# Kernel optimization log

Hardware: AMD Instinct MI355X
Metric: run time of the kernel (lower is better)

The kernel has to match this reference:

```python
import jax, jax.numpy as jnp
import numpy as np

DIM = 1024
S_SIZE = 512
M_SIZE = 4096
L_SIZE = 8192
MERGE_THRESHOLD = 0.98
L_ALPHA = 0.1
K_PROMOTE = max(1, S_SIZE // 4)  # torch: min(len(candidates), max(1, s_size//4)); candidates >> s_size here


def _l2norm(x, axis=-1):
    # F.normalize(p=2) with eps clamp
    return x / jnp.maximum(jnp.linalg.norm(x, axis=axis, keepdims=True), 1e-12)


def _update(processed_tokens, s_memory, m_memory, l_memory, m_utility, l_utility, wq, bq, wk, bk, s_ptr):
    cand = processed_tokens.reshape(-1, DIM)
    # --- S tier: scatter top-k-norm candidates into ring buffer (vectorized; K<=S so slots distinct) ---
    norms = jnp.linalg.norm(cand, axis=1)
    _, top_idx = jax.lax.top_k(norms, K_PROMOTE)
    pos = (s_ptr + jnp.arange(K_PROMOTE)) % S_SIZE
    s_mem = s_memory.at[pos].set(cand[top_idx])
    s_ptr_new = (s_ptr + K_PROMOTE) % S_SIZE
    # --- promotion attention (1 head, only attn weights used): pick best short-term slot ---
    q = l_memory.mean(axis=0) @ wq.T + bq                      # [dim]
    kproj = s_mem @ wk.T + bk                                  # [S, dim]
    attn = jax.nn.softmax(kproj @ q / jnp.sqrt(jnp.asarray(DIM, cand.dtype)))
    best_s_idx = jnp.argmax(attn)
    candidate = s_mem[best_s_idx]                              # [dim]

    # --- M tier: promote / merge / replace ---
    def not_full(mm, mu):
        ridx = jnp.argmin(mu)
        return mm.at[ridx].set(candidate), mu.at[ridx].set(mu.mean() + 1e-5)

    def full(mm, mu):
        mm_norm = _l2norm(mm)
        sims = mm_norm @ _l2norm(candidate)                    # [M]
        msi = jnp.argmax(sims)
        sim_cand = sims[msi]

        def merge_with_candidate(mm, mu):
            merged = _l2norm((mm[msi] + candidate) / 2.0)
            return mm.at[msi].set(merged), mu.at[msi].set((mu[msi] + mu.mean()) / 2.0)

        def try_internal_merge(mm, mu):
            # most redundant pair: strict lower triangle of cosine sim matrix
            sim_mat = mm_norm @ mm_norm.T                      # [M, M]
            sim_mat = jnp.where(jnp.triu(jnp.ones((M_SIZE, M_SIZE), bool)), -1.0, sim_mat)
            flat = jnp.argmax(sim_mat)
            internal_sim = sim_mat.reshape(-1)[flat]
            idx1, idx2 = flat // M_SIZE, flat % M_SIZE

            def do_pair_merge(mm, mu):
                merged = _l2norm((mm[idx1] + mm[idx2]) / 2.0)
                mm2 = mm.at[idx1].set(merged).at[idx2].set(candidate)
                mu1 = mu.at[idx1].set((mu[idx1] + mu[idx2]) / 2.0)
                mu2 = mu1.at[idx2].set(mu1.mean() + 1e-5)      # torch recomputes mean after idx1 write
                return mm2, mu2

            def replace_weakest(mm, mu):
                li = jnp.argmin(mu)
                stronger = jnp.linalg.norm(candidate) > jnp.linalg.norm(mm[li])
                mm2 = jnp.where(stronger, mm.at[li].set(candidate), mm)
                mu2 = jnp.where(stronger, mu.at[li].set(mu.mean() + 1e-5), mu)
                return mm2, mu2

            return jax.lax.cond(internal_sim > MERGE_THRESHOLD, do_pair_merge, replace_weakest, mm, mu)

        return jax.lax.cond(sim_cand > MERGE_THRESHOLD, merge_with_candidate, try_internal_merge, mm, mu)

    is_m_full = ~jnp.any(m_utility == 0)
    m_mem, m_util = jax.lax.cond(is_m_full, full, not_full, m_memory, m_utility)
    # --- L tier: consolidate most-used M slot into least-used L slot ---
    mi = jnp.argmax(m_util)
    lj = jnp.argmin(l_utility)
    consolidated = (1.0 - L_ALPHA) * l_memory[lj] + L_ALPHA * m_mem[mi]
    l_mem = l_memory.at[lj].set(consolidated)
    l_util = l_utility.at[lj].set(l_utility.mean())            # mean of pre-write values
    return s_mem, m_mem, l_mem, m_util, l_util, s_ptr_new


def setup_inputs() -> dict:
    key = jax.random.key(0)
    ks = jax.random.split(key, 10)
    scale = 1.0 / np.sqrt(DIM)
    return {
        "processed_tokens": jax.random.normal(ks[0], (4, 4096, DIM), jnp.float32),
        "s_memory": jax.random.normal(ks[1], (S_SIZE, DIM), jnp.float32),
        "m_memory": jax.random.normal(ks[2], (M_SIZE, DIM), jnp.float32),
        "l_memory": jax.random.normal(ks[3], (L_SIZE, DIM), jnp.float32),
        "m_utility": jax.random.uniform(ks[4], (M_SIZE,), jnp.float32) + 0.01,  # >0 -> 'm full' branch
        "l_utility": jax.random.uniform(ks[5], (L_SIZE,), jnp.float32) + 0.01,
        "wq": jax.random.normal(ks[6], (DIM, DIM), jnp.float32) * scale,
        "bq": jnp.zeros((DIM,), jnp.float32),
        "wk": jax.random.normal(ks[7], (DIM, DIM), jnp.float32) * scale,
        "bk": jnp.zeros((DIM,), jnp.float32),
        "s_ptr": 0,
    }


def reference(processed_tokens, s_memory, m_memory, l_memory, m_utility, l_utility, wq, bq, wk, bk, s_ptr):
    return _update(processed_tokens, s_memory, m_memory, l_memory, m_utility, l_utility, wq, bq, wk, bk, s_ptr)
```

## Files before the change

kernel.cpp:

```cpp
#include <hip/hip_runtime.h>

#define DIMV 1024
#define SSZ 512
#define MSZ 4096
#define LSZ 8192
#define KPROM 128
#define NCAND 16384

typedef __attribute__((ext_vector_type(4))) float f32x4;
typedef __attribute__((ext_vector_type(4))) unsigned int u32x4;
typedef __attribute__((ext_vector_type(4))) unsigned short u16x4;
typedef __attribute__((ext_vector_type(8))) __bf16 bf16x8;

#define OUT_S 0ull
#define OUT_M 524288ull
#define OUT_L 4718592ull
#define OUT_MU 13107200ull
#define OUT_LU 13111296ull
#define OUT_SPTR 13119488ull

#define SC_BF16 0ull
#define SC_NORMS 2100000ull
#define SC_TOPIDX 2117000ull
#define SC_LPART 2120000ull
#define SC_LMEAN 2260000ull
#define SC_Q 2262000ull
#define SC_RPART 2270000ull
#define SC_R 2410000ull
#define SC_CSCAL 2412000ull
#define SC_LOGITS 2413000ull
#define SC_BEST 2414000ull
#define SC_MNORM 2415000ull
#define SC_SIMS 2420000ull
#define SC_PPV 2425000ull
#define SC_PPI 2426000ull
#define SC_DEC 2427000ull

__device__ __forceinline__ float wave_sum(float v) {
#pragma unroll
  for (int o = 32; o > 0; o >>= 1) v += __shfl_down(v, o, 64);
  return v;
}
__device__ __forceinline__ int wave_sum_i(int v) {
#pragma unroll
  for (int o = 32; o > 0; o >>= 1) v += __shfl_down(v, o, 64);
  return v;
}
__device__ __forceinline__ void wave_maxidx(float& v, int& i) {
#pragma unroll
  for (int o = 32; o > 0; o >>= 1) {
    float ov = __shfl_down(v, o, 64);
    int oi = __shfl_down(i, o, 64);
    if (ov > v || (ov == v && oi < i)) { v = ov; i = oi; }
  }
}
__device__ __forceinline__ void wave_minidx(float& v, int& i) {
#pragma unroll
  for (int o = 32; o > 0; o >>= 1) {
    float ov = __shfl_down(v, o, 64);
    int oi = __shfl_down(i, o, 64);
    if (ov < v || (ov == v && oi < i)) { v = ov; i = oi; }
  }
}
__device__ __forceinline__ unsigned short f2bf(float x) {
  unsigned u = __float_as_uint(x);
  return (unsigned short)((u + 0x7FFFu + ((u >> 16) & 1u)) >> 16);
}

__global__ void k_cand_norms(const float* __restrict__ cand, float* __restrict__ norms) {
  int lane = threadIdx.x & 63, w = threadIdx.x >> 6;
  int row = blockIdx.x * 4 + w;
  const f32x4* p = (const f32x4*)(cand + (size_t)row * DIMV);
  float s = 0.f;
#pragma unroll
  for (int c = 0; c < 4; ++c) {
    f32x4 v = p[c * 64 + lane];
    s += v.x * v.x + v.y * v.y + v.z * v.z + v.w * v.w;
  }
  s = wave_sum(s);
  if (lane == 0) norms[row] = sqrtf(s);
}

__device__ int scan_excl_1024(int v, int* sh, int* total) {
  int t = threadIdx.x;
  sh[t] = v;
  __syncthreads();
  for (int o = 1; o < 1024; o <<= 1) {
    int x = (t >= o) ? sh[t - o] : 0;
    __syncthreads();
    sh[t] += x;
    __syncthreads();
  }
  int incl = sh[t];
  *total = sh[1023];
  __syncthreads();
  return incl - v;
}

__global__ void k_topk(const float* __restrict__ norms, int* __restrict__ topidx) {
  __shared__ int sh[1024];
  __shared__ int s_w[16];
  __shared__ int s_tot;
  __shared__ unsigned s_selkey[KPROM];
  __shared__ int s_selidx[KPROM];
  int t = threadIdx.x, lane = t & 63, w = t >> 6;
  unsigned key[16];
#pragma unroll
  for (int j = 0; j < 16; ++j) key[j] = __float_as_uint(norms[t * 16 + j]);

  unsigned prefix = 0;
  int remaining = KPROM;
  for (int bit = 31; bit >= 0; --bit) {
    unsigned himask = (bit == 31) ? 0u : (0xFFFFFFFFu << (bit + 1));
    int c = 0;
#pragma unroll
    for (int j = 0; j < 16; ++j)
      c += (((key[j] & himask) == prefix) && ((key[j] >> bit) & 1u)) ? 1 : 0;
    c = wave_sum_i(c);
    if (lane == 0) s_w[w] = c;
    __syncthreads();
    if (t == 0) {
      int tot = 0;
      for (int i = 0; i < 16; ++i) tot += s_w[i];
      s_tot = tot;
    }
    __syncthreads();
    int tot = s_tot;
    __syncthreads();
    if (tot >= remaining) prefix |= (1u << bit);
    else remaining -= tot;
  }
  unsigned T = prefix;

  int cgt = 0, ceq = 0;
#pragma unroll
  for (int j = 0; j < 16; ++j) { cgt += (key[j] > T); ceq += (key[j] == T); }
  int total_gt, total_eq;
  int sgt = scan_excl_1024(cgt, sh, &total_gt);
  int seq = scan_excl_1024(ceq, sh, &total_eq);
  int need_eq = KPROM - total_gt;
  int g = sgt, e = seq;
#pragma unroll
  for (int j = 0; j < 16; ++j) {
    if (key[j] > T) { s_selkey[g] = key[j]; s_selidx[g] = t * 16 + j; ++g; }
    else if (key[j] == T) {
      if (e < need_eq) { s_selkey[total_gt + e] = key[j]; s_selidx[total_gt + e] = t * 16 + j; }
      ++e;
    }
  }
  __syncthreads();
  if (t < KPROM) {
    unsigned mk = s_selkey[t];
    int mi = s_selidx[t];
    int rank = 0;
    for (int q2 = 0; q2 < KPROM; ++q2) {
      unsigned qk = s_selkey[q2];
      int qi = s_selidx[q2];
      rank += (qk > mk || (qk == mk && qi < mi)) ? 1 : 0;
    }
    topidx[rank] = mi;
  }
}

__global__ void k_write_s(const float* __restrict__ cand, const float* __restrict__ s_memory,
                          const int* __restrict__ topidx, const int* __restrict__ s_ptr,
                          float* __restrict__ out_s, float* __restrict__ out_sptr) {
  int r = blockIdx.x;
  int sp = s_ptr[0];
  int k = (r - sp + SSZ) & (SSZ - 1);
  const float* src = (k < KPROM) ? (cand + (size_t)topidx[k] * DIMV) : (s_memory + (size_t)r * DIMV);
  ((f32x4*)(out_s + (size_t)r * DIMV))[threadIdx.x] = ((const f32x4*)src)[threadIdx.x];
  if (r == 0 && threadIdx.x == 0) out_sptr[0] = (float)((sp + KPROM) % SSZ);
}

__global__ void k_lpart(const float* __restrict__ l_memory, float* __restrict__ lpart) {
  int b = blockIdx.x, t = threadIdx.x;
  f32x4 a = {0.f, 0.f, 0.f, 0.f};
  const f32x4* base = (const f32x4*)(l_memory + (size_t)b * 64 * DIMV);
  for (int r = 0; r < 64; ++r) a += base[r * 256 + t];
  ((f32x4*)(lpart + (size_t)b * DIMV))[t] = a;
}
__global__ void k_lmean(const float* __restrict__ lpart, float* __restrict__ lmean) {
  int c = threadIdx.x;
  f32x4 a = {0.f, 0.f, 0.f, 0.f};
  for (int p = 0; p < 128; ++p) a += ((const f32x4*)lpart)[p * 256 + c];
  ((f32x4*)lmean)[c] = a * (1.f / 8192.f);
}

__global__ void k_q(const float* __restrict__ wq, const float* __restrict__ bq,
                    const float* __restrict__ lmean, float* __restrict__ qv) {
  int lane = threadIdx.x & 63, w = threadIdx.x >> 6;
  int d = blockIdx.x * 4 + w;
  const f32x4* row = (const f32x4*)(wq + (size_t)d * DIMV);
  const f32x4* lm = (const f32x4*)lmean;
  float s = 0.f;
#pragma unroll
  for (int c = 0; c < 4; ++c) {
    f32x4 a = row[c * 64 + lane], b = lm[c * 64 + lane];
    s += a.x * b.x + a.y * b.y + a.z * b.z + a.w * b.w;
  }
  s = wave_sum(s);
  if (lane == 0) qv[d] = s + bq[d];
}

__global__ void k_rpart(const float* __restrict__ wk, const float* __restrict__ qv, float* __restrict__ rpart) {
  int b = blockIdx.x, t = threadIdx.x;
  f32x4 a = {0.f, 0.f, 0.f, 0.f};
  for (int r = 0; r < 8; ++r) {
    float qd = qv[b * 8 + r];
    f32x4 v = ((const f32x4*)(wk + (size_t)(b * 8 + r) * DIMV))[t];
    a += v * qd;
  }
  ((f32x4*)(rpart + (size_t)b * DIMV))[t] = a;
}
__global__ void k_rfinal(const float* __restrict__ rpart, float* __restrict__ rv) {
  int c = threadIdx.x;
  f32x4 a = {0.f, 0.f, 0.f, 0.f};
  for (int p = 0; p < 128; ++p) a += ((const f32x4*)rpart)[p * 256 + c];
  ((f32x4*)rv)[c] = a;
}
__global__ void k_cscal(const float* __restrict__ bk, const float* __restrict__ qv, float* __restrict__ cs) {
  __shared__ float sw[4];
  int lane = threadIdx.x & 63, w = threadIdx.x >> 6;
  f32x4 a = ((const f32x4*)bk)[threadIdx.x];
  f32x4 b = ((const f32x4*)qv)[threadIdx.x];
  float s = a.x * b.x + a.y * b.y + a.z * b.z + a.w * b.w;
  s = wave_sum(s);
  if (lane == 0) sw[w] = s;
  __syncthreads();
  if (threadIdx.x == 0) cs[0] = sw[0] + sw[1] + sw[2] + sw[3];
}

__global__ void k_logits(const float* __restrict__ out_s, const float* __restrict__ rv,
                         const float* __restrict__ cs, float* __restrict__ logits) {
  int lane = threadIdx.x & 63, w = threadIdx.x >> 6;
  int srow = blockIdx.x * 4 + w;
  const f32x4* a = (const f32x4*)(out_s + (size_t)srow * DIMV);
  const f32x4* b = (const f32x4*)rv;
  float s = 0.f;
#pragma unroll
  for (int c = 0; c < 4; ++c) {
    f32x4 x = a[c * 64 + lane], y = b[c * 64 + lane];
    s += x.x * y.x + x.y * y.y + x.z * y.z + x.w * y.w;
  }
  s = wave_sum(s);
  if (lane == 0) logits[srow] = s + cs[0];
}

__global__ void k_argmax_logits(const float* __restrict__ logits, const float* __restrict__ out_s,
                                int* __restrict__ best, float* __restrict__ cnorm) {
  __shared__ float swv[4];
  __shared__ int swi[4];
  int t = threadIdx.x, lane = t & 63, w = t >> 6;
  float v0 = logits[t], v1 = logits[t + 256];
  float bv;
  int bidx;
  if (v1 > v0) { bv = v1; bidx = t + 256; } else { bv = v0; bidx = t; }
  wave_maxidx(bv, bidx);
  if (lane == 0) { swv[w] = bv; swi[w] = bidx; }
  __syncthreads();
  if (t == 0) {
    float a = swv[0]; int ai = swi[0];
    for (int i = 1; i < 4; ++i)
      if (swv[i] > a || (swv[i] == a && swi[i] < ai)) { a = swv[i]; ai = swi[i]; }
    best[0] = ai;
  }
  __syncthreads();
  int bi = best[0];
  f32x4 c4 = ((const f32x4*)(out_s + (size_t)bi * DIMV))[t];
  float s = c4.x * c4.x + c4.y * c4.y + c4.z * c4.z + c4.w * c4.w;
  s = wave_sum(s);
  __syncthreads();
  if (lane == 0) swv[w] = s;
  __syncthreads();
  if (t == 0) cnorm[0] = sqrtf(swv[0] + swv[1] + swv[2] + swv[3]);
}

__global__ void k_msims(const float* __restrict__ m, const float* __restrict__ out_s,
                        const int* __restrict__ best, const float* __restrict__ cnorm,
                        unsigned short* __restrict__ mb, float* __restrict__ mnorm,
                        float* __restrict__ sims) {
  int lane = threadIdx.x & 63, w = threadIdx.x >> 6;
  int row = blockIdx.x * 4 + w;
  const f32x4* mp = (const f32x4*)(m + (size_t)row * DIMV);
  const f32x4* cp = (const f32x4*)(out_s + (size_t)best[0] * DIMV);
  float ss = 0.f, sd = 0.f;
#pragma unroll
  for (int c = 0; c < 4; ++c) {
    int i = c * 64 + lane;
    f32x4 v = mp[i], u = cp[i];
    ss += v.x * v.x + v.y * v.y + v.z * v.z + v.w * v.w;
    sd += v.x * u.x + v.y * u.y + v.z * u.z + v.w * u.w;
    u16x4 h;
    h.x = f2bf(v.x); h.y = f2bf(v.y); h.z = f2bf(v.z); h.w = f2bf(v.w);
    ((u16x4*)(mb + (size_t)row * DIMV))[i] = h;
  }
  ss = wave_sum(ss);
  sd = wave_sum(sd);
  if (lane == 0) {
    float n = sqrtf(ss);
    mnorm[row] = n;
    sims[row] = sd / (fmaxf(n, 1e-12f) * fmaxf(cnorm[0], 1e-12f));
  }
}

__global__ __launch_bounds__(256) void k_pairmax(const unsigned short* __restrict__ mb,
                                                 const float* __restrict__ mnorm,
                                                 float* __restrict__ pv, int* __restrict__ pidx) {
  __shared__ unsigned short At[128 * 72];
  __shared__ unsigned short Bt[128 * 72];
  __shared__ float spv[4];
  __shared__ int spi[4];
  int b = blockIdx.x;
  int bi = 0, acc0 = 0;
  while (acc0 + bi + 1 <= b) { acc0 += bi + 1; ++bi; }
  int bj = b - acc0;
  int t = threadIdx.x, lane = t & 63, w = t >> 6;
  int wr = w >> 1, wc = w & 1;
  int rl = lane & 15, kq = (lane >> 4) * 8, riq = (lane >> 4) * 4;
  int rowA0 = bi * 128, rowB0 = bj * 128;

  f32x4 acc[4][4];
  f32x4 z = {0.f, 0.f, 0.f, 0.f};
#pragma unroll
  for (int i = 0; i < 4; ++i)
#pragma unroll
    for (int j = 0; j < 4; ++j) acc[i][j] = z;

  for (int kc = 0; kc < DIMV; kc += 64) {
    __syncthreads();
#pragma unroll
    for (int c = 0; c < 4; ++c) {
      int chunk = c * 256 + t;
      int r = chunk >> 3, co = (chunk & 7) * 8;
      u32x4 va = *(const u32x4*)(mb + (size_t)(rowA0 + r) * DIMV + kc + co);
      u32x4 vb = *(const u32x4*)(mb + (size_t)(rowB0 + r) * DIMV + kc + co);
      *(u32x4*)(At + r * 72 + co) = va;
      *(u32x4*)(Bt + r * 72 + co) = vb;
    }
    __syncthreads();
#pragma unroll
    for (int ks = 0; ks < 64; ks += 32) {
      bf16x8 af[4], bfv[4];
#pragma unroll
      for (int ti = 0; ti < 4; ++ti)
        af[ti] = *(const bf16x8*)(At + (wr * 64 + ti * 16 + rl) * 72 + ks + kq);
#pragma unroll
      for (int tj = 0; tj < 4; ++tj)
        bfv[tj] = *(const bf16x8*)(Bt + (wc * 64 + tj * 16 + rl) * 72 + ks + kq);
#pragma unroll
      for (int ti = 0; ti < 4; ++ti)
#pragma unroll
        for (int tj = 0; tj < 4; ++tj)
          acc[ti][tj] = __builtin_amdgcn_mfma_f32_16x16x32_bf16(af[ti], bfv[tj], acc[ti][tj], 0, 0, 0);
    }
  }
  float ni[16], nj[4];
#pragma unroll
  for (int ti = 0; ti < 4; ++ti)
#pragma unroll
    for (int r = 0; r < 4; ++r)
      ni[ti * 4 + r] = fmaxf(mnorm[rowA0 + wr * 64 + ti * 16 + riq + r], 1e-12f);
#pragma unroll
  for (int tj = 0; tj < 4; ++tj)
    nj[tj] = fmaxf(mnorm[rowB0 + wc * 64 + tj * 16 + rl], 1e-12f);

  float bv = -3.402823466e38f;
  int bidx = 0x7FFFFFFF;
#pragma unroll
  for (int ti = 0; ti < 4; ++ti)
#pragma unroll
    for (int tj = 0; tj < 4; ++tj)
#pragma unroll
      for (int r = 0; r < 4; ++r) {
        int gi = rowA0 + wr * 64 + ti * 16 + riq + r;
        int gj = rowB0 + wc * 64 + tj * 16 + rl;
        if (gi > gj) {
          float s = acc[ti][tj][r] / (ni[ti * 4 + r] * nj[tj]);
          int fi = gi * MSZ + gj;
          if (s > bv || (s == bv && fi < bidx)) { bv = s; bidx = fi; }
        }
      }
  wave_maxidx(bv, bidx);
  if (lane == 0) { spv[w] = bv; spi[w] = bidx; }
  __syncthreads();
  if (t == 0) {
    float a = spv[0]; int ai = spi[0];
    for (int i = 1; i < 4; ++i)
      if (spv[i] > a || (spv[i] == a && spi[i] < ai)) { a = spv[i]; ai = spi[i]; }
    pv[b] = a;
    pidx[b] = ai;
  }
}

__global__ void k_decide(const float* __restrict__ pv, const int* __restrict__ pidx,
                         const float* __restrict__ sims, const float* __restrict__ mu,
                         const float* __restrict__ mnorm, const float* __restrict__ cnorm,
                         int nblk, int* __restrict__ dec_i, float* __restrict__ dec_f) {
  __shared__ float swv[4];
  __shared__ int swi[4];
  __shared__ float ssum[4];
  __shared__ int szf[4];
  __shared__ float s_res[2];
  __shared__ int s_resi[2];
  int t = threadIdx.x, lane = t & 63, w = t >> 6;

  float bv = -3.402823466e38f;
  int bidx = 0x7FFFFFFF;
  for (int i = t; i < nblk; i += 256) {
    float v = pv[i];
    int fi = pidx[i];
    if (v > bv || (v == bv && fi < bidx)) { bv = v; bidx = fi; }
  }
  wave_maxidx(bv, bidx);
  if (lane == 0) { swv[w] = bv; swi[w] = bidx; }
  __syncthreads();
  if (t == 0) {
    float a = swv[0]; int ai = swi[0];
    for (int i = 1; i < 4; ++i)
      if (swv[i] > a || (swv[i] == a && swi[i] < ai)) { a = swv[i]; ai = swi[i]; }
    s_res[0] = a; s_resi[0] = ai;
  }
  __syncthreads();

  bv = -3.402823466e38f;
  bidx = 0x7FFFFFFF;
#pragma unroll
  for (int j = 0; j < 16; ++j) {
    int i = t * 16 + j;
    float v = sims[i];
    if (v > bv) { bv = v; bidx = i; }
  }
  wave_maxidx(bv, bidx);
  if (lane == 0) { swv[w] = bv; swi[w] = bidx; }
  __syncthreads();
  if (t == 0) {
    float a = swv[0]; int ai = swi[0];
    for (int i = 1; i < 4; ++i)
      if (swv[i] > a || (swv[i] == a && swi[i] < ai)) { a = swv[i]; ai = swi[i]; }
    s_res[1] = a; s_resi[1] = ai;
  }
  __syncthreads();

  float sum = 0.f, mnv = 3.402823466e38f;
  int mni = 0x7FFFFFFF, zf = 0;
#pragma unroll
  for (int j = 0; j < 16; ++j) {
    int i = t * 16 + j;
    float v = mu[i];
    sum += v;
    if (v < mnv) { mnv = v; mni = i; }
    if (v == 0.f) zf = 1;
  }
  sum = wave_sum(sum);
  wave_minidx(mnv, mni);
#pragma unroll
  for (int o = 32; o > 0; o >>= 1) zf |= __shfl_down(zf, o, 64);
  if (lane == 0) { ssum[w] = sum; swv[w] = mnv; swi[w] = mni; szf[w] = zf; }
  __syncthreads();
  if (t == 0) {
    float muSum = ssum[0] + ssum[1] + ssum[2] + ssum[3];
    float a = swv[0]; int li = swi[0];
    for (int i = 1; i < 4; ++i)
      if (swv[i] < a || (swv[i] == a && swi[i] < li)) { a = swv[i]; li = swi[i]; }
    int anyz = szf[0] | szf[1] | szf[2] | szf[3];
    float muMean = muSum / 4096.f;
    float internal_sim = s_res[0];
    int iflat = s_resi[0];
    float sim_cand = s_res[1];
    int msi = s_resi[1];
    int branch, i1 = -1, i2 = -1;
    float u1 = 0.f, u2 = 0.f;
    if (anyz) {
      branch = 0; i1 = li; u1 = muMean + 1e-5f;
    } else if (sim_cand > 0.98f) {
      branch = 1; i1 = msi; u1 = (mu[msi] + muMean) * 0.5f;
    } else if (internal_sim > 0.98f) {
      branch = 2; i1 = iflat / MSZ; i2 = iflat - (iflat / MSZ) * MSZ;
      float o1 = mu[i1], o2 = mu[i2];
      u1 = (o1 + o2) * 0.5f;
      u2 = (muSum - o1 + u1) / 4096.f + 1e-5f;
    } else {
      if (cnorm[0] > mnorm[li]) { branch = 0; i1 = li; u1 = muMean + 1e-5f; }
      else branch = 4;
    }
    dec_i[0] = branch; dec_i[1] = i1; dec_i[2] = i2;
    dec_f[0] = u1; dec_f[1] = u2;
  }
}

__global__ void k_write_m(const float* __restrict__ m, const float* __restrict__ out_s,
                          const int* __restrict__ best, const int* __restrict__ dec_i,
                          float* __restrict__ out_m) {
  __shared__ float sred[4];
  int row = blockIdx.x, t = threadIdx.x, lane = t & 63, w = t >> 6;
  int branch = dec_i[0], i1 = dec_i[1], i2 = dec_i[2];
  int mode = 0;
  if ((branch == 0 && row == i1) || (branch == 2 && row == i2)) mode = 1;
  else if (branch == 1 && row == i1) mode = 2;
  else if (branch == 2 && row == i1) mode = 3;
  f32x4* dst = (f32x4*)(out_m + (size_t)row * DIMV);
  if (mode == 0) {
    dst[t] = ((const f32x4*)(m + (size_t)row * DIMV))[t];
  } else if (mode == 1) {
    dst[t] = ((const f32x4*)(out_s + (size_t)best[0] * DIMV))[t];
  } else {
    f32x4 a = ((const f32x4*)(m + (size_t)row * DIMV))[t];
    f32x4 bb = (mode == 2) ? ((const f32x4*)(out_s + (size_t)best[0] * DIMV))[t]
                           : ((const f32x4*)(m + (size_t)i2 * DIMV))[t];
    f32x4 v = (a + bb) * 0.5f;
    float ss = v.x * v.x + v.y * v.y + v.z * v.z + v.w * v.w;
    ss = wave_sum(ss);
    if (lane == 0) sred[w] = ss;
    __syncthreads();
    float nrm = fmaxf(sqrtf(sred[0] + sred[1] + sred[2] + sred[3]), 1e-12f);
    dst[t] = v / nrm;
  }
}

__global__ void k_write_mu(const float* __restrict__ mu, const int* __restrict__ dec_i,
                           const float* __restrict__ dec_f, float* __restrict__ out_mu) {
  int i = blockIdx.x * 256 + threadIdx.x;
  float v = mu[i];
  int branch = dec_i[0];
  if (branch != 4 && i == dec_i[1]) v = dec_f[0];
  if (branch == 2 && i == dec_i[2]) v = dec_f[1];
  out_mu[i] = v;
}

__global__ void k_ltier(const float* __restrict__ out_mu, const float* __restrict__ lu,
                        float* __restrict__ out_lu, int* __restrict__ wsi) {
  __shared__ float swv[4];
  __shared__ int swi[4];
  __shared__ float ssum[4];
  __shared__ float s_mean;
  __shared__ int s_lj;
  int t = threadIdx.x, lane = t & 63, w = t >> 6;
  float bv = -3.402823466e38f;
  int bidx = 0x7FFFFFFF;
#pragma unroll
  for (int j = 0; j < 16; ++j) {
    int i = t * 16 + j;
    float v = out_mu[i];
    if (v > bv) { bv = v; bidx = i; }
  }
  wave_maxidx(bv, bidx);
  if (lane == 0) { swv[w] = bv; swi[w] = bidx; }
  __syncthreads();
  if (t == 0) {
    float a = swv[0]; int ai = swi[0];
    for (int i = 1; i < 4; ++i)
      if (swv[i] > a || (swv[i] == a && swi[i] < ai)) { a = swv[i]; ai = swi[i]; }
    wsi[1] = ai;
  }
  __syncthreads();
  float mnv = 3.402823466e38f, sum = 0.f;
  int mni = 0x7FFFFFFF;
#pragma unroll
  for (int j = 0; j < 32; ++j) {
    int i = t * 32 + j;
    float v = lu[i];
    sum += v;
    if (v < mnv) { mnv = v; mni = i; }
  }
  sum = wave_sum(sum);
  wave_minidx(mnv, mni);
  if (lane == 0) { swv[w] = mnv; swi[w] = mni; ssum[w] = sum; }
  __syncthreads();
  if (t == 0) {
    float a = swv[0]; int ai = swi[0];
    for (int i = 1; i < 4; ++i)
      if (swv[i] < a || (swv[i] == a && swi[i] < ai)) { a = swv[i]; ai = swi[i]; }
    s_lj = ai;
    s_mean = (ssum[0] + ssum[1] + ssum[2] + ssum[3]) / 8192.f;
    wsi[0] = ai;
  }
  __syncthreads();
  int lj = s_lj;
  float lmv = s_mean;
#pragma unroll
  for (int j = 0; j < 32; ++j) {
    int i = t * 32 + j;
    out_lu[i] = (i == lj) ? lmv : lu[i];
  }
}

__global__ void k_write_l(const float* __restrict__ l_memory, const float* __restrict__ out_m,
                          const int* __restrict__ wsi, float* __restrict__ out_l) {
  int row = blockIdx.x, t = threadIdx.x;
  int lj = wsi[0], mi = wsi[1];
  f32x4 v = ((const f32x4*)(l_memory + (size_t)row * DIMV))[t];
  if (row == lj) {
    f32x4 mv = ((const f32x4*)(out_m + (size_t)mi * DIMV))[t];
    v = v * 0.9f + mv * 0.1f;
  }
  ((f32x4*)(out_l + (size_t)row * DIMV))[t] = v;
}

extern "C" void kernel_launch(void* const* d_in, const int* in_sizes, int n_in,
                              void* d_out, int out_size, void* d_ws, size_t ws_size,
                              hipStream_t stream) {
  const float* cand = (const float*)d_in[0];
  const float* s_memory = (const float*)d_in[1];
  const float* m_memory = (const float*)d_in[2];
  const float* l_memory = (const float*)d_in[3];
  const float* m_utility = (const float*)d_in[4];
  const float* l_utility = (const float*)d_in[5];
  const float* wq = (const float*)d_in[6];
  const float* bq = (const float*)d_in[7];
  const float* wk = (const float*)d_in[8];
  const float* bk = (const float*)d_in[9];
  const int* s_ptr = (const int*)d_in[10];

  float* out = (float*)d_out;
  float* out_s = out + OUT_S;
  float* out_m = out + OUT_M;
  float* out_l = out + OUT_L;
  float* out_mu = out + OUT_MU;
  float* out_lu = out + OUT_LU;
  float* out_sptr = out + OUT_SPTR;

  float* lsc = out_l;
  unsigned short* mb = (unsigned short*)(lsc + SC_BF16);
  float* norms = lsc + SC_NORMS;
  int* topidx = (int*)(lsc + SC_TOPIDX);
  float* lpart = lsc + SC_LPART;
  float* lmean = lsc + SC_LMEAN;
  float* qv = lsc + SC_Q;
  float* rpart = lsc + SC_RPART;
  float* rv = lsc + SC_R;
  float* cs = lsc + SC_CSCAL;
  float* logits = lsc + SC_LOGITS;
  int* best = (int*)(lsc + SC_BEST);
  float* cnorm = lsc + SC_BEST + 1;
  float* mnorm = lsc + SC_MNORM;
  float* sims = lsc + SC_SIMS;
  float* pv = lsc + SC_PPV;
  int* pidx = (int*)(lsc + SC_PPI);
  int* dec_i = (int*)(lsc + SC_DEC);
  float* dec_f = lsc + SC_DEC + 4;
  int* wsi = (int*)d_ws;

  k_cand_norms<<<4096, 256, 0, stream>>>(cand, norms);
  k_topk<<<1, 1024, 0, stream>>>(norms, topidx);
  k_write_s<<<512, 256, 0, stream>>>(cand, s_memory, topidx, s_ptr, out_s, out_sptr);
  k_lpart<<<128, 256, 0, stream>>>(l_memory, lpart);
  k_lmean<<<1, 256, 0, stream>>>(lpart, lmean);
  k_q<<<256, 256, 0, stream>>>(wq, bq, lmean, qv);
  k_rpart<<<128, 256, 0, stream>>>(wk, qv, rpart);
  k_rfinal<<<1, 256, 0, stream>>>(rpart, rv);
  k_cscal<<<1, 256, 0, stream>>>(bk, qv, cs);
  k_logits<<<128, 256, 0, stream>>>(out_s, rv, cs, logits);
  k_argmax_logits<<<1, 256, 0, stream>>>(logits, out_s, best, cnorm);
  k_msims<<<1024, 256, 0, stream>>>(m_memory, out_s, best, cnorm, mb, mnorm, sims);
  k_pairmax<<<528, 256, 0, stream>>>(mb, mnorm, pv, pidx);
  k_decide<<<1, 256, 0, stream>>>(pv, pidx, sims, m_utility, mnorm, cnorm, 528, dec_i, dec_f);
  k_write_m<<<4096, 256, 0, stream>>>(m_memory, out_s, best, dec_i, out_m);
  k_write_mu<<<16, 256, 0, stream>>>(m_utility, dec_i, dec_f, out_mu);
  k_ltier<<<1, 256, 0, stream>>>(out_mu, l_utility, out_lu, wsi);
  k_write_l<<<8192, 256, 0, stream>>>(l_memory, out_m, wsi, out_l);
}
```

Baseline: 332.1 us.

## Merge launch chain into fewer multi-role kernels and retile pair-similarity GEMM

New measurement: 327.0 us. No clear change (-1.5%).

```diff
diff --git a/kernel.cpp b/kernel.cpp
--- a/kernel.cpp
+++ b/kernel.cpp
@@ -6,6 +6,7 @@
 #define LSZ 8192
 #define KPROM 128
 #define NCAND 16384
+#define NPAIR 1056
 
 typedef __attribute__((ext_vector_type(4))) float f32x4;
 typedef __attribute__((ext_vector_type(4))) unsigned int u32x4;
@@ -23,25 +24,17 @@
 #define SC_NORMS 2100000ull
 #define SC_TOPIDX 2117000ull
 #define SC_LPART 2120000ull
-#define SC_LMEAN 2260000ull
-#define SC_Q 2262000ull
-#define SC_RPART 2270000ull
-#define SC_R 2410000ull
-#define SC_CSCAL 2412000ull
+#define SC_RV 2260000ull
+#define SC_LMEAN 2262000ull
+#define SC_Q 2264000ull
 #define SC_LOGITS 2413000ull
 #define SC_BEST 2414000ull
 #define SC_MNORM 2415000ull
 #define SC_SIMS 2420000ull
 #define SC_PPV 2425000ull
-#define SC_PPI 2426000ull
-#define SC_DEC 2427000ull
+#define SC_PPI 2427000ull
 
 __device__ __forceinline__ float wave_sum(float v) {
-#pragma unroll
-  for (int o = 32; o > 0; o >>= 1) v += __shfl_down(v, o, 64);
-  return v;
-}
-__device__ __forceinline__ int wave_sum_i(int v) {
 #pragma unroll
   for (int o = 32; o > 0; o >>= 1) v += __shfl_down(v, o, 64);
   return v;
@@ -67,18 +60,44 @@
   return (unsigned short)((u + 0x7FFFu + ((u >> 16) & 1u)) >> 16);
 }
 
-__global__ void k_cand_norms(const float* __restrict__ cand, float* __restrict__ norms) {
-  int lane = threadIdx.x & 63, w = threadIdx.x >> 6;
-  int row = blockIdx.x * 4 + w;
-  const f32x4* p = (const f32x4*)(cand + (size_t)row * DIMV);
-  float s = 0.f;
-#pragma unroll
-  for (int c = 0; c < 4; ++c) {
-    f32x4 v = p[c * 64 + lane];
-    s += v.x * v.x + v.y * v.y + v.z * v.z + v.w * v.w;
-  }
-  s = wave_sum(s);
-  if (lane == 0) norms[row] = sqrtf(s);
+__global__ void kA(const float* __restrict__ cand, const float* __restrict__ l_memory,
+                   const float* __restrict__ m, float* __restrict__ norms,
+                   float* __restrict__ lpart, unsigned short* __restrict__ mb,
+                   float* __restrict__ mnorm) {
+  int b = blockIdx.x, t = threadIdx.x, lane = t & 63, w = t >> 6;
+  if (b < 4096) {
+    int row = b * 4 + w;
+    const f32x4* p = (const f32x4*)(cand + (size_t)row * DIMV);
+    float s = 0.f;
+#pragma unroll
+    for (int c = 0; c < 4; ++c) {
+      f32x4 v = p[c * 64 + lane];
+      s += v.x * v.x + v.y * v.y + v.z * v.z + v.w * v.w;
+    }
+    s = wave_sum(s);
+    if (lane == 0) norms[row] = sqrtf(s);
+  } else if (b < 4224) {
+    int bb = b - 4096;
+    f32x4 a = {0.f, 0.f, 0.f, 0.f};
+    const f32x4* base = (const f32x4*)(l_memory + (size_t)bb * 64 * DIMV);
+    for (int r = 0; r < 64; ++r) a += base[r * 256 + t];
+    ((f32x4*)(lpart + (size_t)bb * DIMV))[t] = a;
+  } else {
+    int row = (b - 4224) * 4 + w;
+    const f32x4* mp = (const f32x4*)(m + (size_t)row * DIMV);
+    float ss = 0.f;
+#pragma unroll
+    for (int c = 0; c < 4; ++c) {
+      int i = c * 64 + lane;
+      f32x4 v = mp[i];
+      ss += v.x * v.x + v.y * v.y + v.z * v.z + v.w * v.w;
+      u16x4 h;
+      h.x = f2bf(v.x); h.y = f2bf(v.y); h.z = f2bf(v.z); h.w = f2bf(v.w);
+      ((u16x4*)(mb + (size_t)row * DIMV))[i] = h;
+    }
+    ss = wave_sum(ss);
+    if (lane == 0) mnorm[row] = sqrtf(ss);
+  }
 }
 
 __device__ int scan_excl_1024(int v, int* sh, int* total) {
@@ -97,38 +116,50 @@
   return incl - v;
 }
 
-__global__ void k_topk(const float* __restrict__ norms, int* __restrict__ topidx) {
+__global__ void kT(const float* __restrict__ norms, int* __restrict__ topidx,
+                   const float* __restrict__ lpart, float* __restrict__ lmean) {
+  int t = threadIdx.x;
+  if (blockIdx.x == 1) {
+    float s = 0.f;
+    for (int p = 0; p < 128; ++p) s += lpart[(size_t)p * DIMV + t];
+    lmean[t] = s * (1.f / 8192.f);
+    return;
+  }
   __shared__ int sh[1024];
-  __shared__ int s_w[16];
-  __shared__ int s_tot;
+  __shared__ int hist[256];
   __shared__ unsigned s_selkey[KPROM];
   __shared__ int s_selidx[KPROM];
-  int t = threadIdx.x, lane = t & 63, w = t >> 6;
+  __shared__ int s_digit, s_sub;
   unsigned key[16];
 #pragma unroll
   for (int j = 0; j < 16; ++j) key[j] = __float_as_uint(norms[t * 16 + j]);
 
-  unsigned prefix = 0;
+  unsigned prefix = 0, himask = 0;
   int remaining = KPROM;
-  for (int bit = 31; bit >= 0; --bit) {
-    unsigned himask = (bit == 31) ? 0u : (0xFFFFFFFFu << (bit + 1));
-    int c = 0;
+  for (int p = 24; p >= 0; p -= 8) {
+    if (t < 256) hist[t] = 0;
+    __syncthreads();
 #pragma unroll
     for (int j = 0; j < 16; ++j)
-      c += (((key[j] & himask) == prefix) && ((key[j] >> bit) & 1u)) ? 1 : 0;
-    c = wave_sum_i(c);
-    if (lane == 0) s_w[w] = c;
-    __syncthreads();
-    if (t == 0) {
-      int tot = 0;
-      for (int i = 0; i < 16; ++i) tot += s_w[i];
-      s_tot = tot;
-    }
-    __syncthreads();
-    int tot = s_tot;
-    __syncthreads();
-    if (tot >= remaining) prefix |= (1u << bit);
-    else remaining -= tot;
+      if ((key[j] & himask) == prefix) atomicAdd(&hist[(key[j] >> p) & 255], 1);
+    __syncthreads();
+    if (t < 256) sh[t] = hist[t];
+    __syncthreads();
+    for (int o = 1; o < 256; o <<= 1) {
+      int x = (t < 256 && t + o < 256) ? sh[t + o] : 0;
+      __syncthreads();
+      if (t < 256) sh[t] += x;
+      __syncthreads();
+    }
+    if (t < 256) {
+      int sfex = (t < 255) ? sh[t + 1] : 0;
+      if (sfex < remaining && remaining <= sh[t]) { s_digit = t; s_sub = sfex; }
+    }
+    __syncthreads();
+    prefix |= ((unsigned)s_digit) << p;
+    remaining -= s_sub;
+    himask |= (0xFFu << p);
+    __syncthreads();
   }
   unsigned T = prefix;
 
@@ -162,48 +193,36 @@
   }
 }
 
-__global__ void k_write_s(const float* __restrict__ cand, const float* __restrict__ s_memory,
-                          const int* __restrict__ topidx, const int* __restrict__ s_ptr,
-                          float* __restrict__ out_s, float* __restrict__ out_sptr) {
-  int r = blockIdx.x;
-  int sp = s_ptr[0];
-  int k = (r - sp + SSZ) & (SSZ - 1);
-  const float* src = (k < KPROM) ? (cand + (size_t)topidx[k] * DIMV) : (s_memory + (size_t)r * DIMV);
-  ((f32x4*)(out_s + (size_t)r * DIMV))[threadIdx.x] = ((const f32x4*)src)[threadIdx.x];
-  if (r == 0 && threadIdx.x == 0) out_sptr[0] = (float)((sp + KPROM) % SSZ);
-}
-
-__global__ void k_lpart(const float* __restrict__ l_memory, float* __restrict__ lpart) {
+__global__ void kB(const float* __restrict__ cand, const float* __restrict__ s_memory,
+                   const int* __restrict__ topidx, const int* __restrict__ s_ptr,
+                   const float* __restrict__ wq, const float* __restrict__ bq,
+                   const float* __restrict__ lmean, float* __restrict__ out_s,
+                   float* __restrict__ out_sptr, float* __restrict__ qv) {
   int b = blockIdx.x, t = threadIdx.x;
-  f32x4 a = {0.f, 0.f, 0.f, 0.f};
-  const f32x4* base = (const f32x4*)(l_memory + (size_t)b * 64 * DIMV);
-  for (int r = 0; r < 64; ++r) a += base[r * 256 + t];
-  ((f32x4*)(lpart + (size_t)b * DIMV))[t] = a;
-}
-__global__ void k_lmean(const float* __restrict__ lpart, float* __restrict__ lmean) {
-  int c = threadIdx.x;
-  f32x4 a = {0.f, 0.f, 0.f, 0.f};
-  for (int p = 0; p < 128; ++p) a += ((const f32x4*)lpart)[p * 256 + c];
-  ((f32x4*)lmean)[c] = a * (1.f / 8192.f);
-}
-
-__global__ void k_q(const float* __restrict__ wq, const float* __restrict__ bq,
-                    const float* __restrict__ lmean, float* __restrict__ qv) {
-  int lane = threadIdx.x & 63, w = threadIdx.x >> 6;
-  int d = blockIdx.x * 4 + w;
-  const f32x4* row = (const f32x4*)(wq + (size_t)d * DIMV);
-  const f32x4* lm = (const f32x4*)lmean;
-  float s = 0.f;
-#pragma unroll
-  for (int c = 0; c < 4; ++c) {
-    f32x4 a = row[c * 64 + lane], b = lm[c * 64 + lane];
-    s += a.x * b.x + a.y * b.y + a.z * b.z + a.w * b.w;
-  }
-  s = wave_sum(s);
-  if (lane == 0) qv[d] = s + bq[d];
-}
-
-__global__ void k_rpart(const float* __restrict__ wk, const float* __restrict__ qv, float* __restrict__ rpart) {
+  if (b < 512) {
+    int sp = s_ptr[0];
+    int k = (b - sp + SSZ) & (SSZ - 1);
+    const float* src = (k < KPROM) ? (cand + (size_t)topidx[k] * DIMV) : (s_memory + (size_t)b * DIMV);
+    ((f32x4*)(out_s + (size_t)b * DIMV))[t] = ((const f32x4*)src)[t];
+    if (b == 0 && t == 0) out_sptr[0] = (float)((sp + KPROM) % SSZ);
+  } else {
+    int lane = t & 63, w = t >> 6;
+    int d = (b - 512) * 4 + w;
+    const f32x4* row = (const f32x4*)(wq + (size_t)d * DIMV);
+    const f32x4* lm = (const f32x4*)lmean;
+    float s = 0.f;
+#pragma unroll
+    for (int c = 0; c < 4; ++c) {
+      f32x4 a = row[c * 64 + lane], bb = lm[c * 64 + lane];
+      s += a.x * bb.x + a.y * bb.y + a.z * bb.z + a.w * bb.w;
+    }
+    s = wave_sum(s);
+    if (lane == 0) qv[d] = s + bq[d];
+  }
+}
+
+__global__ void kC(const float* __restrict__ wk, const float* __restrict__ qv,
+                   float* __restrict__ rv) {
   int b = blockIdx.x, t = threadIdx.x;
   f32x4 a = {0.f, 0.f, 0.f, 0.f};
   for (int r = 0; r < 8; ++r) {
@@ -211,28 +230,14 @@
     f32x4 v = ((const f32x4*)(wk + (size_t)(b * 8 + r) * DIMV))[t];
     a += v * qd;
   }
-  ((f32x4*)(rpart + (size_t)b * DIMV))[t] = a;
-}
-__global__ void k_rfinal(const float* __restrict__ rpart, float* __restrict__ rv) {
-  int c = threadIdx.x;
-  f32x4 a = {0.f, 0.f, 0.f, 0.f};
-  for (int p = 0; p < 128; ++p) a += ((const f32x4*)rpart)[p * 256 + c];
-  ((f32x4*)rv)[c] = a;
-}
-__global__ void k_cscal(const float* __restrict__ bk, const float* __restrict__ qv, float* __restrict__ cs) {
-  __shared__ float sw[4];
-  int lane = threadIdx.x & 63, w = threadIdx.x >> 6;
-  f32x4 a = ((const f32x4*)bk)[threadIdx.x];
-  f32x4 b = ((const f32x4*)qv)[threadIdx.x];
-  float s = a.x * b.x + a.y * b.y + a.z * b.z + a.w * b.w;
-  s = wave_sum(s);
-  if (lane == 0) sw[w] = s;
-  __syncthreads();
-  if (threadIdx.x == 0) cs[0] = sw[0] + sw[1] + sw[2] + sw[3];
-}
-
-__global__ void k_logits(const float* __restrict__ out_s, const float* __restrict__ rv,
-                         const float* __restrict__ cs, float* __restrict__ logits) {
+  atomicAdd(&rv[t * 4 + 0], a.x);
+  atomicAdd(&rv[t * 4 + 1], a.y);
+  atomicAdd(&rv[t * 4 + 2], a.z);
+  atomicAdd(&rv[t * 4 + 3], a.w);
+}
+
+__global__ void kD(const float* __restrict__ out_s, const float* __restrict__ rv,
+                   float* __restrict__ logits) {
   int lane = threadIdx.x & 63, w = threadIdx.x >> 6;
   int srow = blockIdx.x * 4 + w;
   const f32x4* a = (const f32x4*)(out_s + (size_t)srow * DIMV);
@@ -244,11 +249,11 @@
     s += x.x * y.x + x.y * y.y + x.z * y.z + x.w * y.w;
   }
   s = wave_sum(s);
-  if (lane == 0) logits[srow] = s + cs[0];
-}
-
-__global__ void k_argmax_logits(const float* __restrict__ logits, const float* __restrict__ out_s,
-                                int* __restrict__ best, float* __restrict__ cnorm) {
+  if (lane == 0) logits[srow] = s;
+}
+
+__global__ void kE(const float* __restrict__ logits, const float* __restrict__ out_s,
+                   int* __restrict__ best, float* __restrict__ cnorm) {
   __shared__ float swv[4];
   __shared__ int swi[4];
   int t = threadIdx.x, lane = t & 63, w = t >> 6;
@@ -276,105 +281,100 @@
   if (t == 0) cnorm[0] = sqrtf(swv[0] + swv[1] + swv[2] + swv[3]);
 }
 
-__global__ void k_msims(const float* __restrict__ m, const float* __restrict__ out_s,
-                        const int* __restrict__ best, const float* __restrict__ cnorm,
-                        unsigned short* __restrict__ mb, float* __restrict__ mnorm,
-                        float* __restrict__ sims) {
-  int lane = threadIdx.x & 63, w = threadIdx.x >> 6;
-  int row = blockIdx.x * 4 + w;
-  const f32x4* mp = (const f32x4*)(m + (size_t)row * DIMV);
-  const f32x4* cp = (const f32x4*)(out_s + (size_t)best[0] * DIMV);
-  float ss = 0.f, sd = 0.f;
-#pragma unroll
-  for (int c = 0; c < 4; ++c) {
-    int i = c * 64 + lane;
-    f32x4 v = mp[i], u = cp[i];
-    ss += v.x * v.x + v.y * v.y + v.z * v.z + v.w * v.w;
-    sd += v.x * u.x + v.y * u.y + v.z * u.z + v.w * u.w;
-    u16x4 h;
-    h.x = f2bf(v.x); h.y = f2bf(v.y); h.z = f2bf(v.z); h.w = f2bf(v.w);
-    ((u16x4*)(mb + (size_t)row * DIMV))[i] = h;
-  }
-  ss = wave_sum(ss);
-  sd = wave_sum(sd);
-  if (lane == 0) {
-    float n = sqrtf(ss);
-    mnorm[row] = n;
-    sims[row] = sd / (fmaxf(n, 1e-12f) * fmaxf(cnorm[0], 1e-12f));
-  }
-}
-
-__global__ __launch_bounds__(256) void k_pairmax(const unsigned short* __restrict__ mb,
-                                                 const float* __restrict__ mnorm,
-                                                 float* __restrict__ pv, int* __restrict__ pidx) {
+__global__ __launch_bounds__(256, 4) void kG(const unsigned short* __restrict__ mb,
+                                             const float* __restrict__ mnorm,
+                                             const float* __restrict__ m,
+                                             const float* __restrict__ out_s,
+                                             const int* __restrict__ best,
+                                             const float* __restrict__ cnorm,
+                                             float* __restrict__ pv, int* __restrict__ pidx,
+                                             float* __restrict__ sims) {
+  int b = blockIdx.x, t = threadIdx.x, lane = t & 63, w = t >> 6;
+  if (b >= NPAIR) {
+    int row = (b - NPAIR) * 4 + w;
+    const f32x4* mp = (const f32x4*)(m + (size_t)row * DIMV);
+    const f32x4* cp = (const f32x4*)(out_s + (size_t)best[0] * DIMV);
+    float sd = 0.f;
+#pragma unroll
+    for (int c = 0; c < 4; ++c) {
+      int i = c * 64 + lane;
+      f32x4 v = mp[i], u = cp[i];
+      sd += v.x * u.x + v.y * u.y + v.z * u.z + v.w * u.w;
+    }
+    sd = wave_sum(sd);
+    if (lane == 0) sims[row] = sd / (fmaxf(mnorm[row], 1e-12f) * fmaxf(cnorm[0], 1e-12f));
+    return;
+  }
   __shared__ unsigned short At[128 * 72];
-  __shared__ unsigned short Bt[128 * 72];
+  __shared__ unsigned short Bt[64 * 72];
   __shared__ float spv[4];
   __shared__ int spi[4];
-  int b = blockIdx.x;
-  int bi = 0, acc0 = 0;
-  while (acc0 + bi + 1 <= b) { acc0 += bi + 1; ++bi; }
-  int bj = b - acc0;
-  int t = threadIdx.x, lane = t & 63, w = t >> 6;
+  int bi = (int)((sqrtf(4.f * (float)b + 1.f) - 1.f) * 0.5f);
+  while (bi * bi + bi > b) --bi;
+  while ((bi + 1) * (bi + 1) + (bi + 1) <= b) ++bi;
+  int bj = b - (bi * bi + bi);
   int wr = w >> 1, wc = w & 1;
   int rl = lane & 15, kq = (lane >> 4) * 8, riq = (lane >> 4) * 4;
-  int rowA0 = bi * 128, rowB0 = bj * 128;
-
-  f32x4 acc[4][4];
+  int rowA0 = bi * 128, rowB0 = bj * 64;
+
+  f32x4 acc[4][2];
   f32x4 z = {0.f, 0.f, 0.f, 0.f};
 #pragma unroll
-  for (int i = 0; i < 4; ++i)
-#pragma unroll
-    for (int j = 0; j < 4; ++j) acc[i][j] = z;
+  for (int i = 0; i < 4; ++i) { acc[i][0] = z; acc[i][1] = z; }
 
   for (int kc = 0; kc < DIMV; kc += 64) {
     __syncthreads();
 #pragma unroll
-    for (int c = 0; c < 4; ++c) {
+    for (int c = 0; c < 6; ++c) {
       int chunk = c * 256 + t;
-      int r = chunk >> 3, co = (chunk & 7) * 8;
-      u32x4 va = *(const u32x4*)(mb + (size_t)(rowA0 + r) * DIMV + kc + co);
-      u32x4 vb = *(const u32x4*)(mb + (size_t)(rowB0 + r) * DIMV + kc + co);
-      *(u32x4*)(At + r * 72 + co) = va;
-      *(u32x4*)(Bt + r * 72 + co) = vb;
+      if (chunk < 1024) {
+        int r = chunk >> 3, g = chunk & 7;
+        u32x4 va = *(const u32x4*)(mb + (size_t)(rowA0 + r) * DIMV + kc + g * 8);
+        *(u32x4*)(At + r * 72 + g * 8) = va;
+      } else {
+        int c3 = chunk - 1024;
+        int r = c3 >> 3, g = c3 & 7;
+        u32x4 vb = *(const u32x4*)(mb + (size_t)(rowB0 + r) * DIMV + kc + g * 8);
+        *(u32x4*)(Bt + r * 72 + g * 8) = vb;
+      }
     }
     __syncthreads();
 #pragma unroll
     for (int ks = 0; ks < 64; ks += 32) {
-      bf16x8 af[4], bfv[4];
+      bf16x8 af[4], bfv[2];
 #pragma unroll
       for (int ti = 0; ti < 4; ++ti)
         af[ti] = *(const bf16x8*)(At + (wr * 64 + ti * 16 + rl) * 72 + ks + kq);
 #pragma unroll
-      for (int tj = 0; tj < 4; ++tj)
-        bfv[tj] = *(const bf16x8*)(Bt + (wc * 64 + tj * 16 + rl) * 72 + ks + kq);
+      for (int tj = 0; tj < 2; ++tj)
+        bfv[tj] = *(const bf16x8*)(Bt + (wc * 32 + tj * 16 + rl) * 72 + ks + kq);
 #pragma unroll
       for (int ti = 0; ti < 4; ++ti)
 #pragma unroll
-        for (int tj = 0; tj < 4; ++tj)
+        for (int tj = 0; tj < 2; ++tj)
           acc[ti][tj] = __builtin_amdgcn_mfma_f32_16x16x32_bf16(af[ti], bfv[tj], acc[ti][tj], 0, 0, 0);
     }
   }
-  float ni[16], nj[4];
+  float ni[16], nj[2];
 #pragma unroll
   for (int ti = 0; ti < 4; ++ti)
 #pragma unroll
     for (int r = 0; r < 4; ++r)
       ni[ti * 4 + r] = fmaxf(mnorm[rowA0 + wr * 64 + ti * 16 + riq + r], 1e-12f);
 #pragma unroll
-  for (int tj = 0; tj < 4; ++tj)
-    nj[tj] = fmaxf(mnorm[rowB0 + wc * 64 + tj * 16 + rl], 1e-12f);
+  for (int tj = 0; tj < 2; ++tj)
+    nj[tj] = fmaxf(mnorm[rowB0 + wc * 32 + tj * 16 + rl], 1e-12f);
 
   float bv = -3.402823466e38f;
   int bidx = 0x7FFFFFFF;
 #pragma unroll
   for (int ti = 0; ti < 4; ++ti)
 #pragma unroll
-    for (int tj = 0; tj < 4; ++tj)
+    for (int tj = 0; tj < 2; ++tj)
 #pragma unroll
       for (int r = 0; r < 4; ++r) {
         int gi = rowA0 + wr * 64 + ti * 16 + riq + r;
-        int gj = rowB0 + wc * 64 + tj * 16 + rl;
+        int gj = rowB0 + wc * 32 + tj * 16 + rl;
         if (gi > gj) {
           float s = acc[ti][tj][r] / (ni[ti * 4 + r] * nj[tj]);
           int fi = gi * MSZ + gj;
@@ -393,21 +393,25 @@
   }
 }
 
-__global__ void k_decide(const float* __restrict__ pv, const int* __restrict__ pidx,
-                         const float* __restrict__ sims, const float* __restrict__ mu,
-                         const float* __restrict__ mnorm, const float* __restrict__ cnorm,
-                         int nblk, int* __restrict__ dec_i, float* __restrict__ dec_f) {
-  __shared__ float swv[4];
-  __shared__ int swi[4];
-  __shared__ float ssum[4];
-  __shared__ int szf[4];
+__global__ void kH(const float* __restrict__ pv, const int* __restrict__ pidx,
+                   const float* __restrict__ sims, const float* __restrict__ mu,
+                   const float* __restrict__ mnorm, const float* __restrict__ cnorm,
+                   const int* __restrict__ best, const float* __restrict__ lu,
+                   float* __restrict__ out_mu, float* __restrict__ out_lu,
+                   int* __restrict__ ws) {
+  __shared__ float swv[16];
+  __shared__ int swi[16];
+  __shared__ float ssum[16];
+  __shared__ int szf[16];
   __shared__ float s_res[2];
   __shared__ int s_resi[2];
+  __shared__ int s_branch, s_i1, s_i2, s_lj;
+  __shared__ float s_u1, s_u2, s_lmean;
   int t = threadIdx.x, lane = t & 63, w = t >> 6;
 
   float bv = -3.402823466e38f;
   int bidx = 0x7FFFFFFF;
-  for (int i = t; i < nblk; i += 256) {
+  for (int i = t; i < NPAIR; i += 1024) {
     float v = pv[i];
     int fi = pidx[i];
     if (v > bv || (v == bv && fi < bidx)) { bv = v; bidx = fi; }
@@ -417,7 +421,7 @@
   __syncthreads();
   if (t == 0) {
     float a = swv[0]; int ai = swi[0];
-    for (int i = 1; i < 4; ++i)
+    for (int i = 1; i < 16; ++i)
       if (swv[i] > a || (swv[i] == a && swi[i] < ai)) { a = swv[i]; ai = swi[i]; }
     s_res[0] = a; s_resi[0] = ai;
   }
@@ -426,8 +430,8 @@
   bv = -3.402823466e38f;
   bidx = 0x7FFFFFFF;
 #pragma unroll
-  for (int j = 0; j < 16; ++j) {
-    int i = t * 16 + j;
+  for (int j = 0; j < 4; ++j) {
+    int i = t * 4 + j;
     float v = sims[i];
     if (v > bv) { bv = v; bidx = i; }
   }
@@ -436,18 +440,20 @@
   __syncthreads();
   if (t == 0) {
     float a = swv[0]; int ai = swi[0];
-    for (int i = 1; i < 4; ++i)
+    for (int i = 1; i < 16; ++i)
       if (swv[i] > a || (swv[i] == a && swi[i] < ai)) { a = swv[i]; ai = swi[i]; }
     s_res[1] = a; s_resi[1] = ai;
   }
   __syncthreads();
 
+  float muv[4];
   float sum = 0.f, mnv = 3.402823466e38f;
   int mni = 0x7FFFFFFF, zf = 0;
 #pragma unroll
-  for (int j = 0; j < 16; ++j) {
-    int i = t * 16 + j;
+  for (int j = 0; j < 4; ++j) {
+    int i = t * 4 + j;
     float v = mu[i];
+    muv[j] = v;
     sum += v;
     if (v < mnv) { mnv = v; mni = i; }
     if (v == 0.f) zf = 1;
@@ -459,11 +465,14 @@
   if (lane == 0) { ssum[w] = sum; swv[w] = mnv; swi[w] = mni; szf[w] = zf; }
   __syncthreads();
   if (t == 0) {
-    float muSum = ssum[0] + ssum[1] + ssum[2] + ssum[3];
+    float muSum = 0.f;
+    int anyz = 0;
     float a = swv[0]; int li = swi[0];
-    for (int i = 1; i < 4; ++i)
-      if (swv[i] < a || (swv[i] == a && swi[i] < li)) { a = swv[i]; li = swi[i]; }
-    int anyz = szf[0] | szf[1] | szf[2] | szf[3];
+    for (int i = 0; i < 16; ++i) {
+      muSum += ssum[i];
+      anyz |= szf[i];
+      if (i > 0 && (swv[i] < a || (swv[i] == a && swi[i] < li))) { a = swv[i]; li = swi[i]; }
+    }
     float muMean = muSum / 4096.f;
     float internal_sim = s_res[0];
     int iflat = s_resi[0];
@@ -484,117 +493,129 @@
       if (cnorm[0] > mnorm[li]) { branch = 0; i1 = li; u1 = muMean + 1e-5f; }
       else branch = 4;
     }
-    dec_i[0] = branch; dec_i[1] = i1; dec_i[2] = i2;
-    dec_f[0] = u1; dec_f[1] = u2;
-  }
-}
-
-__global__ void k_write_m(const float* __restrict__ m, const float* __restrict__ out_s,
-                          const int* __restrict__ best, const int* __restrict__ dec_i,
-                          float* __restrict__ out_m) {
-  __shared__ float sred[4];
-  int row = blockIdx.x, t = threadIdx.x, lane = t & 63, w = t >> 6;
-  int branch = dec_i[0], i1 = dec_i[1], i2 = dec_i[2];
-  int mode = 0;
-  if ((branch == 0 && row == i1) || (branch == 2 && row == i2)) mode = 1;
-  else if (branch == 1 && row == i1) mode = 2;
-  else if (branch == 2 && row == i1) mode = 3;
-  f32x4* dst = (f32x4*)(out_m + (size_t)row * DIMV);
-  if (mode == 0) {
-    dst[t] = ((const f32x4*)(m + (size_t)row * DIMV))[t];
-  } else if (mode == 1) {
-    dst[t] = ((const f32x4*)(out_s + (size_t)best[0] * DIMV))[t];
-  } else {
-    f32x4 a = ((const f32x4*)(m + (size_t)row * DIMV))[t];
-    f32x4 bb = (mode == 2) ? ((const f32x4*)(out_s + (size_t)best[0] * DIMV))[t]
-                           : ((const f32x4*)(m + (size_t)i2 * DIMV))[t];
-    f32x4 v = (a + bb) * 0.5f;
-    float ss = v.x * v.x + v.y * v.y + v.z * v.z + v.w * v.w;
-    ss = wave_sum(ss);
-    if (lane == 0) sred[w] = ss;
-    __syncthreads();
-    float nrm = fmaxf(sqrtf(sred[0] + sred[1] + sred[2] + sred[3]), 1e-12f);
-    dst[t] = v / nrm;
-  }
-}
-
-__global__ void k_write_mu(const float* __restrict__ mu, const int* __restrict__ dec_i,
-                           const float* __restrict__ dec_f, float* __restrict__ out_mu) {
-  int i = blockIdx.x * 256 + threadIdx.x;
-  float v = mu[i];
-  int branch = dec_i[0];
-  if (branch != 4 && i == dec_i[1]) v = dec_f[0];
-  if (branch == 2 && i == dec_i[2]) v = dec_f[1];
-  out_mu[i] = v;
-}
-
-__global__ void k_ltier(const float* __restrict__ out_mu, const float* __restrict__ lu,
-                        float* __restrict__ out_lu, int* __restrict__ wsi) {
-  __shared__ float swv[4];
-  __shared__ int swi[4];
-  __shared__ float ssum[4];
-  __shared__ float s_mean;
-  __shared__ int s_lj;
-  int t = threadIdx.x, lane = t & 63, w = t >> 6;
-  float bv = -3.402823466e38f;
-  int bidx = 0x7FFFFFFF;
-#pragma unroll
-  for (int j = 0; j < 16; ++j) {
-    int i = t * 16 + j;
-    float v = out_mu[i];
+    s_branch = branch; s_i1 = i1; s_i2 = i2; s_u1 = u1; s_u2 = u2;
+    ws[2] = branch; ws[3] = i1; ws[4] = i2; ws[5] = best[0];
+  }
+  __syncthreads();
+
+  int branch = s_branch, i1 = s_i1, i2 = s_i2;
+  float u1 = s_u1, u2 = s_u2;
+  bv = -3.402823466e38f;
+  bidx = 0x7FFFFFFF;
+#pragma unroll
+  for (int j = 0; j < 4; ++j) {
+    int i = t * 4 + j;
+    float v = muv[j];
+    if (branch != 4 && i == i1) v = u1;
+    if (branch == 2 && i == i2) v = u2;
+    out_mu[i] = v;
     if (v > bv) { bv = v; bidx = i; }
   }
   wave_maxidx(bv, bidx);
+  __syncthreads();
   if (lane == 0) { swv[w] = bv; swi[w] = bidx; }
   __syncthreads();
   if (t == 0) {
     float a = swv[0]; int ai = swi[0];
-    for (int i = 1; i < 4; ++i)
+    for (int i = 1; i < 16; ++i)
       if (swv[i] > a || (swv[i] == a && swi[i] < ai)) { a = swv[i]; ai = swi[i]; }
-    wsi[1] = ai;
-  }
-  __syncthreads();
-  float mnv = 3.402823466e38f, sum = 0.f;
-  int mni = 0x7FFFFFFF;
-#pragma unroll
-  for (int j = 0; j < 32; ++j) {
-    int i = t * 32 + j;
+    ws[1] = ai;
+  }
+
+  float luv[8];
+  sum = 0.f; mnv = 3.402823466e38f; mni = 0x7FFFFFFF;
+#pragma unroll
+  for (int j = 0; j < 8; ++j) {
+    int i = t * 8 + j;
     float v = lu[i];
+    luv[j] = v;
     sum += v;
     if (v < mnv) { mnv = v; mni = i; }
   }
   sum = wave_sum(sum);
   wave_minidx(mnv, mni);
+  __syncthreads();
   if (lane == 0) { swv[w] = mnv; swi[w] = mni; ssum[w] = sum; }
   __syncthreads();
   if (t == 0) {
     float a = swv[0]; int ai = swi[0];
-    for (int i = 1; i < 4; ++i)
-      if (swv[i] < a || (swv[i] == a && swi[i] < ai)) { a = swv[i]; ai = swi[i]; }
+    float ls = 0.f;
+    for (int i = 0; i < 16; ++i) {
+      ls += ssum[i];
+      if (i > 0 && (swv[i] < a || (swv[i] == a && swi[i] < ai))) { a = swv[i]; ai = swi[i]; }
+    }
     s_lj = ai;
-    s_mean = (ssum[0] + ssum[1] + ssum[2] + ssum[3]) / 8192.f;
-    wsi[0] = ai;
+    s_lmean = ls / 8192.f;
+    ws[0] = ai;
   }
   __syncthreads();
   int lj = s_lj;
-  float lmv = s_mean;
-#pragma unroll
-  for (int j = 0; j < 32; ++j) {
-    int i = t * 32 + j;
-    out_lu[i] = (i == lj) ? lmv : lu[i];
-  }
-}
-
-__global__ void k_write_l(const float* __restrict__ l_memory, const float* __restrict__ out_m,
-                          const int* __restrict__ wsi, float* __restrict__ out_l) {
-  int row = blockIdx.x, t = threadIdx.x;
-  int lj = wsi[0], mi = wsi[1];
-  f32x4 v = ((const f32x4*)(l_memory + (size_t)row * DIMV))[t];
-  if (row == lj) {
-    f32x4 mv = ((const f32x4*)(out_m + (size_t)mi * DIMV))[t];
-    v = v * 0.9f + mv * 0.1f;
-  }
-  ((f32x4*)(out_l + (size_t)row * DIMV))[t] = v;
+  float lmv = s_lmean;
+#pragma unroll
+  for (int j = 0; j < 8; ++j) {
+    int i = t * 8 + j;
+    out_lu[i] = (i == lj) ? lmv : luv[j];
+  }
+}
+
+__global__ void kI(const float* __restrict__ m, const float* __restrict__ l_memory,
+                   const float* __restrict__ out_s, const int* __restrict__ ws,
+                   float* __restrict__ out_m, float* __restrict__ out_l) {
+  __shared__ float sred[4];
+  int b = blockIdx.x, t = threadIdx.x, lane = t & 63, w = t >> 6;
+  int lj = ws[0], mi = ws[1], branch = ws[2], i1 = ws[3], i2 = ws[4], best = ws[5];
+  if (b < 4096) {
+    int row = b;
+    int mode = 0;
+    if ((branch == 0 && row == i1) || (branch == 2 && row == i2)) mode = 1;
+    else if (branch == 1 && row == i1) mode = 2;
+    else if (branch == 2 && row == i1) mode = 3;
+    f32x4* dst = (f32x4*)(out_m + (size_t)row * DIMV);
+    if (mode == 0) {
+      dst[t] = ((const f32x4*)(m + (size_t)row * DIMV))[t];
+    } else if (mode == 1) {
+      dst[t] = ((const f32x4*)(out_s + (size_t)best * DIMV))[t];
+    } else {
+      f32x4 a = ((const f32x4*)(m + (size_t)row * DIMV))[t];
+      f32x4 bb = (mode == 2) ? ((const f32x4*)(out_s + (size_t)best * DIMV))[t]
+                             : ((const f32x4*)(m + (size_t)i2 * DIMV))[t];
+      f32x4 v = (a + bb) * 0.5f;
+      float ss = v.x * v.x + v.y * v.y + v.z * v.z + v.w * v.w;
+      ss = wave_sum(ss);
+      if (lane == 0) sred[w] = ss;
+      __syncthreads();
+      float nrm = fmaxf(sqrtf(sred[0] + sred[1] + sred[2] + sred[3]), 1e-12f);
+      dst[t] = v / nrm;
+    }
+  } else {
+    int row = b - 4096;
+    f32x4 v = ((const f32x4*)(l_memory + (size_t)row * DIMV))[t];
+    if (row == lj) {
+      int mode = 0;
+      if ((branch == 0 && mi == i1) || (branch == 2 && mi == i2)) mode = 1;
+      else if (branch == 1 && mi == i1) mode = 2;
+      else if (branch == 2 && mi == i1) mode = 3;
+      f32x4 mv;
+      if (mode == 0) {
+        mv = ((const f32x4*)(m + (size_t)mi * DIMV))[t];
+      } else if (mode == 1) {
+        mv = ((const f32x4*)(out_s + (size_t)best * DIMV))[t];
+      } else {
+        f32x4 a = ((const f32x4*)(m + (size_t)mi * DIMV))[t];
+        f32x4 bb = (mode == 2) ? ((const f32x4*)(out_s + (size_t)best * DIMV))[t]
+                               : ((const f32x4*)(m + (size_t)i2 * DIMV))[t];
+        f32x4 vm = (a + bb) * 0.5f;
+        float ss = vm.x * vm.x + vm.y * vm.y + vm.z * vm.z + vm.w * vm.w;
+        ss = wave_sum(ss);
+        if (lane == 0) sred[w] = ss;
+        __syncthreads();
+        float nrm = fmaxf(sqrtf(sred[0] + sred[1] + sred[2] + sred[3]), 1e-12f);
+        mv = vm / nrm;
+      }
+      v = v * 0.9f + mv * 0.1f;
+    }
+    ((f32x4*)(out_l + (size_t)row * DIMV))[t] = v;
+  }
 }
 
 extern "C" void kernel_launch(void* const* d_in, const int* in_sizes, int n_in,
@@ -611,6 +632,7 @@
   const float* wk = (const float*)d_in[8];
   const float* bk = (const float*)d_in[9];
   const int* s_ptr = (const int*)d_in[10];
+  (void)bk;
 
   float* out = (float*)d_out;
   float* out_s = out + OUT_S;
@@ -625,11 +647,9 @@
   float* norms = lsc + SC_NORMS;
   int* topidx = (int*)(lsc + SC_TOPIDX);
   float* lpart = lsc + SC_LPART;
+  float* rv = lsc + SC_RV;
   float* lmean = lsc + SC_LMEAN;
   float* qv = lsc + SC_Q;
-  float* rpart = lsc + SC_RPART;
-  float* rv = lsc + SC_R;
-  float* cs = lsc + SC_CSCAL;
   float* logits = lsc + SC_LOGITS;
   int* best = (int*)(lsc + SC_BEST);
   float* cnorm = lsc + SC_BEST + 1;
@@ -637,26 +657,17 @@
   float* sims = lsc + SC_SIMS;
   float* pv = lsc + SC_PPV;
   int* pidx = (int*)(lsc + SC_PPI);
-  int* dec_i = (int*)(lsc + SC_DEC);
-  float* dec_f = lsc + SC_DEC + 4;
-  int* wsi = (int*)d_ws;
-
-  k_cand_norms<<<4096, 256, 0, stream>>>(cand, norms);
-  k_topk<<<1, 1024, 0, stream>>>(norms, topidx);
-  k_write_s<<<512, 256, 0, stream>>>(cand, s_memory, topidx, s_ptr, out_s, out_sptr);
-  k_lpart<<<128, 256, 0, stream>>>(l_memory, lpart);
-  k_lmean<<<1, 256, 0, stream>>>(lpart, lmean);
-  k_q<<<256, 256, 0, stream>>>(wq, bq, lmean, qv);
-  k_rpart<<<128, 256, 0, stream>>>(wk, qv, rpart);
-  k_rfinal<<<1, 256, 0, stream>>>(rpart, rv);
-  k_cscal<<<1, 256, 0, stream>>>(bk, qv, cs);
-  k_logits<<<128, 256, 0, stream>>>(out_s, rv, cs, logits);
-  k_argmax_logits<<<1, 256, 0, stream>>>(logits, out_s, best, cnorm);
-  k_msims<<<1024, 256, 0, stream>>>(m_memory, out_s, best, cnorm, mb, mnorm, sims);
-  k_pairmax<<<528, 256, 0, stream>>>(mb, mnorm, pv, pidx);
-  k_decide<<<1, 256, 0, stream>>>(pv, pidx, sims, m_utility, mnorm, cnorm, 528, dec_i, dec_f);
-  k_write_m<<<4096, 256, 0, stream>>>(m_memory, out_s, best, dec_i, out_m);
-  k_write_mu<<<16, 256, 0, stream>>>(m_utility, dec_i, dec_f, out_mu);
-  k_ltier<<<1, 256, 0, stream>>>(out_mu, l_utility, out_lu, wsi);
-  k_write_l<<<8192, 256, 0, stream>>>(l_memory, out_m, wsi, out_l);
-}
+  int* wsctl = (int*)d_ws;
+
+  hipMemsetAsync(rv, 0, 4096, stream);
+  kA<<<5248, 256, 0, stream>>>(cand, l_memory, m_memory, norms, lpart, mb, mnorm);
+  kT<<<2, 1024, 0, stream>>>(norms, topidx, lpart, lmean);
+  kB<<<768, 256, 0, stream>>>(cand, s_memory, topidx, s_ptr, wq, bq, lmean, out_s, out_sptr, qv);
+  kC<<<128, 256, 0, stream>>>(wk, qv, rv);
+  kD<<<128, 256, 0, stream>>>(out_s, rv, logits);
+  kE<<<1, 256, 0, stream>>>(logits, out_s, best, cnorm);
+  kG<<<NPAIR + 1024, 256, 0, stream>>>(mb, mnorm, m_memory, out_s, best, cnorm, pv, pidx, sims);
+  kH<<<1, 1024, 0, stream>>>(pv, pidx, sims, m_utility, mnorm, cnorm, best, l_utility,
+                             out_mu, out_lu, wsctl);
+  kI<<<12288, 256, 0, stream>>>(m_memory, l_memory, out_s, wsctl, out_m, out_l);
+}
```
